# Optimization experiments

Hardware: AMD Instinct MI355X
Metric: run time of the kernel (lower is better)

Reference implementation:

```python
import jax, jax.numpy as jnp
import numpy as np

# 24 directional shifts (dy, dx): out[h,w] = in[h-dy, w-dx], zero elsewhere.
SHIFTS = [(0,1),(0,-1),(1,0),(-1,0),(1,1),(-1,-1),(1,-1),(-1,1),
          (0,2),(0,-2),(2,0),(-2,0),(2,2),(-2,-2),(2,-2),(-2,2),
          (2,1),(1,2),(2,-1),(1,-2),(-2,1),(-1,2),(-2,-1),(-1,-2)]

def shift2d(xg, dy, dx):
    B, G, H, W = xg.shape
    pt, pb = max(dy,0), max(-dy,0)
    pl, pr = max(dx,0), max(-dx,0)
    xp = jnp.pad(xg, ((0,0),(0,0),(pt,pb),(pl,pr)))
    return xp[:, :, pb:pb+H, pr:pr+W]

def mul_shift(x4, gamma=1.0/24.0):
    B, C, H, W = x4.shape
    g = int(C * gamma)
    parts = [shift2d(x4[:, i*g:(i+1)*g], dy, dx) for i, (dy, dx) in enumerate(SHIFTS)]
    parts.append(x4[:, 24*g:])
    return jnp.concatenate(parts, axis=1)

def zigzag_indices(h, w, start='top-left', direction='horizontal'):
    if start == 'top-left':   row_start, col_start, row_step, col_step = 0, 0, 1, 1
    elif start == 'top-right': row_start, col_start, row_step, col_step = 0, w-1, 1, -1
    elif start == 'bottom-left': row_start, col_start, row_step, col_step = h-1, 0, -1, 1
    else:                     row_start, col_start, row_step, col_step = h-1, w-1, -1, -1
    idx = []
    for i in range(h):
        r = row_start + row_step * i
        if direction == 'horizontal':
            cols = range(w) if r % 2 == 0 else range(w-1, -1, -1)
            idx += [r * w + c for c in cols]
        else:
            cc = col_start + col_step * i
            rows = range(h) if cc % 2 == 0 else range(h-1, -1, -1)
            idx += [rr * w + cc for rr in rows]
    return np.asarray(idx, dtype=np.int32)

def wkv(w, u, k, v):
    """Numerically stable RWKV WKV recurrence. w,u:(C,) k,v:(B,T,C) -> (B,T,C)."""
    B, T, C = k.shape
    def step(carry, kv):
        p, q, o = carry
        kt, vt = kv
        no = jnp.maximum(o, u + kt)
        A = jnp.exp(o - no); Bc = jnp.exp(u + kt - no)
        y = (A * p + Bc * vt) / (A * q + Bc)
        no2 = jnp.maximum(w + o, kt)
        A2 = jnp.exp(w + o - no2); B2 = jnp.exp(kt - no2)
        return (A2 * p + B2 * vt, A2 * q + B2, no2), y
    init = (jnp.zeros((B, C), k.dtype), jnp.zeros((B, C), k.dtype),
            jnp.full((B, C), -1e38, k.dtype))
    _, ys = jax.lax.scan(step, init, (jnp.swapaxes(k, 0, 1), jnp.swapaxes(v, 0, 1)))
    return jnp.swapaxes(ys, 0, 1)

def setup_inputs() -> dict:
    key = jax.random.key(0)
    ks = jax.random.split(key, 8)
    B, H, W, C = 8, 64, 64, 768
    scale = 0.02
    return {
        'x': jax.random.normal(ks[0], (B, H*W, C), jnp.float32),
        'key_w': jax.random.normal(ks[1], (C, C), jnp.float32) * scale,
        'value_w': jax.random.normal(ks[2], (C, C), jnp.float32) * scale,
        'receptance_w': jax.random.normal(ks[3], (C, C), jnp.float32) * scale,
        'output_w': jax.random.normal(ks[4], (C, C), jnp.float32) * scale,
        'spatial_decay': jax.random.normal(ks[5], (2, C), jnp.float32),
        'spatial_first': jax.random.normal(ks[6], (2, C), jnp.float32),
        'h': H, 'w': W,
    }

def reference(x, key_w, value_w, receptance_w, output_w, spatial_decay, spatial_first, h, w):
    B, T, C = x.shape
    # layer_id=0 -> scheme ('top-left','horizontal')
    order = jnp.asarray(zigzag_indices(h, w, 'top-left', 'horizontal'))
    inv = jnp.argsort(order)
    # jit_func: mul_shift in (B,C,H,W), zigzag reorder along T, projections
    x4 = jnp.transpose(x.reshape(B, h, w, C), (0, 3, 1, 2))
    x4 = mul_shift(x4)
    xs = jnp.transpose(x4.reshape(B, C, T)[:, :, order], (0, 2, 1))  # (B,T,C)
    k = xs @ key_w.T
    v = xs @ value_w.T
    sr = jax.nn.sigmoid(xs @ receptance_w.T)
    # recurrence j=0
    v = wkv(spatial_decay[0] / T, spatial_first[0] / T, k, v)
    # recurrence j=1: zigzag-permute, WKV, inverse-permute (horizontal -> same grid)
    k2 = k[:, order]
    v2 = v[:, order]
    v2 = wkv(spatial_decay[1] / T, spatial_first[1] / T, k2, v2)
    v = v2[:, inv]
    return (sr * v) @ output_w.T
```

## Files before the change

kernel.cpp:

```cpp
#include <hip/hip_runtime.h>
#include <hip/hip_bf16.h>
#include <hip/hip_fp16.h>

#define T_SEQ 4096
#define CDIM  768
#define BDIM  8
#define MROWS (BDIM * T_SEQ)
#define NKVR  (3 * CDIM)
#define CHL   64
#define NCH   (T_SEQ / CHL)
#define BC    (BDIM * CDIM)

typedef __attribute__((ext_vector_type(8))) short   short8;
typedef __attribute__((ext_vector_type(4))) float   floatx4;
typedef unsigned short ushort_t;
struct ushort4_t { ushort_t x, y, z, w; };

__device__ __forceinline__ ushort_t f2b(float f) {
    __hip_bfloat16 h = __float2bfloat16(f);
    return *(ushort_t*)&h;
}
__device__ __forceinline__ float b2f(ushort_t s) {
    __hip_bfloat16 h;
    *(ushort_t*)&h = s;
    return __bfloat162float(h);
}
__device__ __forceinline__ ushort_t f2h(float f) {
    __half h = __float2half(f);
    return *(ushort_t*)&h;
}
__device__ __forceinline__ float h2f(ushort_t s) {
    __half h;
    *(ushort_t*)&h = s;
    return __half2float(h);
}

__device__ __forceinline__ void gload_lds16(const void* g, void* l) {
    __builtin_amdgcn_global_load_lds(
        (const __attribute__((address_space(1))) void*)g,
        (__attribute__((address_space(3))) void*)l, 16, 0, 0);
}

__constant__ int c_dy[24] = {0,0,1,-1,1,-1,1,-1,0,0,2,-2,2,-2,2,-2,2,1,2,1,-2,-1,-2,-1};
__constant__ int c_dx[24] = {1,-1,0,0,1,-1,-1,1,2,-2,0,0,2,-2,-2,2,1,2,-1,-2,1,2,-1,-2};

__global__ void cvt_weights(const float* __restrict__ kw, const float* __restrict__ vw,
                            const float* __restrict__ rw, const float* __restrict__ ow,
                            ushort_t* __restrict__ wkvr, ushort_t* __restrict__ wo) {
    int i = blockIdx.x * 256 + threadIdx.x;
    if (i < CDIM * CDIM) {
        wkvr[i]                   = f2b(kw[i]);
        wkvr[i + CDIM * CDIM]     = f2b(vw[i]);
        wkvr[i + 2 * CDIM * CDIM] = f2b(rw[i]);
        wo[i]                     = f2b(ow[i]);
    }
}

__global__ void shift_zigzag(const float* __restrict__ x, ushort_t* __restrict__ xs) {
    size_t i = (size_t)blockIdx.x * 256 + threadIdx.x;
    if (i >= (size_t)MROWS * (CDIM / 4)) return;
    int c4 = (int)(i % (CDIM / 4)) * 4;
    size_t bt = i / (CDIM / 4);
    int tz = (int)(bt % T_SEQ);
    int b  = (int)(bt / T_SEQ);
    int r = tz >> 6, pos = tz & 63;
    int xcol = (r & 1) ? (63 - pos) : pos;
    int g = c4 >> 5;
    int ys = r - c_dy[g];
    int xsrc = xcol - c_dx[g];
    float4 val = {0.f, 0.f, 0.f, 0.f};
    if ((unsigned)ys < 64u && (unsigned)xsrc < 64u)
        val = *(const float4*)(x + ((size_t)b * T_SEQ + (size_t)(ys * 64 + xsrc)) * CDIM + c4);
    ushort4_t o;
    o.x = f2b(val.x); o.y = f2b(val.y); o.z = f2b(val.z); o.w = f2b(val.w);
    *(ushort4_t*)(xs + bt * CDIM + c4) = o;
}

template <int MODE, int NB>
__global__ __launch_bounds__(256, 3) void gemm_bt(
    const ushort_t* __restrict__ A, const ushort_t* __restrict__ Bw,
    ushort_t* __restrict__ out_k, ushort_t* __restrict__ out_v,
    ushort_t* __restrict__ out_sr, float* __restrict__ out_f) {
    __shared__ ushort_t As[128 * 32];
    __shared__ ushort_t Bs[128 * 32];
    const int p    = blockIdx.x;
    const int xcd  = p & 7;
    const int s    = p >> 3;
    const int mb   = xcd + 8 * (s / NB);
    const int nb   = s % NB;
    const int m0   = mb * 128;
    const int n0   = nb * 128;
    const int t    = threadIdx.x;
    const int lane = t & 63;
    const int wv   = t >> 6;
    const int wm   = (wv & 1) * 64;
    const int wn   = (wv >> 1) * 64;
    const int srow = t >> 2;
    const int skc  = (t & 3) ^ ((srow >> 1) & 3);
    const int kb   = skc * 8;
    const int l15  = lane & 15;
    const int l4   = lane >> 4;

    floatx4 acc[4][4];
#pragma unroll
    for (int i = 0; i < 4; i++)
#pragma unroll
        for (int j = 0; j < 4; j++) acc[i][j] = (floatx4){0.f, 0.f, 0.f, 0.f};

    for (int kk = 0; kk < CDIM; kk += 32) {
        __syncthreads();
        gload_lds16(A  + (size_t)(m0 + srow)      * CDIM + kk + kb, (void*)(As + t * 8));
        gload_lds16(A  + (size_t)(m0 + 64 + srow) * CDIM + kk + kb, (void*)(As + 2048 + t * 8));
        gload_lds16(Bw + (size_t)(n0 + srow)      * CDIM + kk + kb, (void*)(Bs + t * 8));
        gload_lds16(Bw + (size_t)(n0 + 64 + srow) * CDIM + kk + kb, (void*)(Bs + 2048 + t * 8));
        __syncthreads();
        short8 af[4], bfv[4];
#pragma unroll
        for (int mi = 0; mi < 4; mi++) {
            int ra = wm + mi * 16 + l15;
            af[mi] = *(const short8*)(As + ra * 32 + ((l4 ^ ((ra >> 1) & 3)) << 3));
        }
#pragma unroll
        for (int ni = 0; ni < 4; ni++) {
            int rb = wn + ni * 16 + l15;
            bfv[ni] = *(const short8*)(Bs + rb * 32 + ((l4 ^ ((rb >> 1) & 3)) << 3));
        }
#pragma unroll
        for (int mi = 0; mi < 4; mi++)
#pragma unroll
            for (int ni = 0; ni < 4; ni++)
                acc[mi][ni] = __builtin_amdgcn_mfma_f32_16x16x32_bf16(
                    af[mi], bfv[ni], acc[mi][ni], 0, 0, 0);
    }

    const int region = (MODE == 0) ? (nb / 6) : 0;
    ushort_t* outh = (region == 0) ? out_k : (region == 1) ? out_v : out_sr;
    const int ncb = n0 - region * CDIM;
#pragma unroll
    for (int mi = 0; mi < 4; mi++) {
#pragma unroll
        for (int ni = 0; ni < 4; ni++) {
            int nc = ncb + wn + ni * 16 + l15;
#pragma unroll
            for (int r = 0; r < 4; r++) {
                int mg = m0 + wm + mi * 16 + l4 * 4 + r;
                float val = acc[mi][ni][r];
                if (MODE == 0) {
                    if (region < 2)
                        outh[(size_t)mg * CDIM + nc] = f2h(val);
                    else
                        outh[(size_t)mg * CDIM + nc] =
                            f2b(1.0f / (1.0f + __expf(-val)));
                } else {
                    out_f[(size_t)mg * CDIM + (n0 + wn + ni * 16 + l15)] = val;
                }
            }
        }
    }
}


__global__ __launch_bounds__(256) void wkv_chunk_sum0(
    const ushort_t* __restrict__ kbuf, const ushort_t* __restrict__ vbuf,
    const float* __restrict__ sd,
    float* __restrict__ sumP, float* __restrict__ sumQ, float* __restrict__ sumO) {
    int gid = blockIdx.x * 256 + threadIdx.x;
    int bc = gid % BC;
    int ch = gid / BC;
    int b = bc / CDIM, c = bc % CDIM;
    const float w = sd[c] * (1.0f / (float)T_SEQ);
    size_t base = (size_t)b * T_SEQ * CDIM + c + (size_t)ch * CHL * CDIM;
    float p = 0.f, q = 0.f, o = -1e38f;
#pragma unroll 4
    for (int i = 0; i < CHL; i++) {
        size_t off = base + (size_t)i * CDIM;
        float kt = h2f(kbuf[off]), vt = h2f(vbuf[off]);
        float wo_ = w + o;
        float no2 = fmaxf(wo_, kt);
        float A2 = __expf(wo_ - no2), B2 = __expf(kt - no2);
        p = A2 * p + B2 * vt;
        q = A2 * q + B2;
        o = no2;
    }
    size_t idx = (size_t)ch * BC + bc;
    sumP[idx] = p; sumQ[idx] = q; sumO[idx] = o;
}

__global__ __launch_bounds__(256) void wkv_chunk_scan(
    const float* __restrict__ sumP, const float* __restrict__ sumQ,
    const float* __restrict__ sumO,
    float* __restrict__ inP, float* __restrict__ inQ, float* __restrict__ inO,
    const float* __restrict__ sd, int pass) {
    int bc = blockIdx.x * 256 + threadIdx.x;
    if (bc >= BC) return;
    int c = bc % CDIM;
    const float w = sd[pass * CDIM + c] * (1.0f / (float)T_SEQ);
    const float Lw = w * (float)CHL;
    float p = 0.f, q = 0.f, o = -1e38f;
    for (int ch = 0; ch < NCH; ch++) {
        size_t idx = (size_t)ch * BC + bc;
        inP[idx] = p; inQ[idx] = q; inO[idx] = o;
        float Pc = sumP[idx], Qc = sumQ[idx], Oc = sumO[idx];
        float ow_ = o + Lw;
        float no = fmaxf(ow_, Oc);
        float e1 = __expf(ow_ - no), e2 = __expf(Oc - no);
        p = e1 * p + e2 * Pc;
        q = e1 * q + e2 * Qc;
        o = no;
    }
}

__global__ __launch_bounds__(256) void wkv_replay0_sum1(
    const ushort_t* __restrict__ kbuf, ushort_t* __restrict__ vbuf,
    const float* __restrict__ sd, const float* __restrict__ sf,
    const float* __restrict__ inP, const float* __restrict__ inQ,
    const float* __restrict__ inO,
    float* __restrict__ sumP, float* __restrict__ sumQ, float* __restrict__ sumO) {
    int gid = blockIdx.x * 256 + threadIdx.x;
    int bc = gid % BC;
    int ch = gid / BC;
    int b = bc / CDIM, c = bc % CDIM;
    const float w1 = sd[c] * (1.0f / (float)T_SEQ);
    const float u1 = sf[c] * (1.0f / (float)T_SEQ);
    size_t base = (size_t)b * T_SEQ * CDIM + c + (size_t)ch * CHL * CDIM;
    size_t idx = (size_t)ch * BC + bc;
    float p = inP[idx], q = inQ[idx], o = inO[idx];
    float yv[CHL];
    float kv[CHL];
#pragma unroll 4
    for (int i = 0; i < CHL; i++) {
        size_t off = base + (size_t)i * CDIM;
        float kt = h2f(kbuf[off]), vt = h2f(vbuf[off]);
        kv[i] = kt;
        float uk = u1 + kt;
        float no = fmaxf(o, uk);
        float Ae = __expf(o - no), Be = __expf(uk - no);
        float y = (Ae * p + Be * vt) / (Ae * q + Be);
        float wo_ = w1 + o;
        float no2 = fmaxf(wo_, kt);
        float A2 = __expf(wo_ - no2), B2 = __expf(kt - no2);
        p = A2 * p + B2 * vt;
        q = A2 * q + B2;
        o = no2;
        yv[i] = y;
        vbuf[off] = f2h(y);
    }
    const float w2 = sd[CDIM + c] * (1.0f / (float)T_SEQ);
    float p2 = 0.f, q2 = 0.f, o2 = -1e38f;
    if (ch & 1) {
#pragma unroll 4
        for (int i = CHL - 1; i >= 0; i--) {
            float kt = kv[i], vt = yv[i];
            float wo_ = w2 + o2;
            float no2 = fmaxf(wo_, kt);
            float A2 = __expf(wo_ - no2), B2 = __expf(kt - no2);
            p2 = A2 * p2 + B2 * vt;
            q2 = A2 * q2 + B2;
            o2 = no2;
        }
    } else {
#pragma unroll 4
        for (int i = 0; i < CHL; i++) {
            float kt = kv[i], vt = yv[i];
            float wo_ = w2 + o2;
            float no2 = fmaxf(wo_, kt);
            float A2 = __expf(wo_ - no2), B2 = __expf(kt - no2);
            p2 = A2 * p2 + B2 * vt;
            q2 = A2 * q2 + B2;
            o2 = no2;
        }
    }
    sumP[idx] = p2; sumQ[idx] = q2; sumO[idx] = o2;
}

__global__ __launch_bounds__(256) void wkv_replay1(
    const ushort_t* __restrict__ kbuf, const ushort_t* __restrict__ vbuf,
    const ushort_t* __restrict__ srb, ushort_t* __restrict__ a2,
    const float* __restrict__ sd, const float* __restrict__ sf,
    const float* __restrict__ inP, const float* __restrict__ inQ,
    const float* __restrict__ inO) {
    int gid = blockIdx.x * 256 + threadIdx.x;
    int bc = gid % BC;
    int ch = gid / BC;
    int b = bc / CDIM, c = bc % CDIM;
    const float w = sd[CDIM + c] * (1.0f / (float)T_SEQ);
    const float u = sf[CDIM + c] * (1.0f / (float)T_SEQ);
    size_t base = (size_t)b * T_SEQ * CDIM + c;
    size_t idx = (size_t)ch * BC + bc;
    float p = inP[idx], q = inQ[idx], o = inO[idx];
#pragma unroll 4
    for (int i = 0; i < CHL; i++) {
        int row = ch * CHL + ((ch & 1) ? (CHL - 1 - i) : i);
        size_t off = base + (size_t)row * CDIM;
        float kt = h2f(kbuf[off]), vt = h2f(vbuf[off]);
        float uk = u + kt;
        float no = fmaxf(o, uk);
        float Ae = __expf(o - no), Be = __expf(uk - no);
        float y = (Ae * p + Be * vt) / (Ae * q + Be);
        float wo_ = w + o;
        float no2 = fmaxf(wo_, kt);
        float A2 = __expf(wo_ - no2), B2 = __expf(kt - no2);
        p = A2 * p + B2 * vt;
        q = A2 * q + B2;
        o = no2;
        a2[off] = f2b(y * b2f(srb[off]));
    }
}

extern "C" void kernel_launch(void* const* d_in, const int* in_sizes, int n_in,
                              void* d_out, int out_size, void* d_ws, size_t ws_size,
                              hipStream_t stream) {
    (void)in_sizes; (void)n_in; (void)out_size; (void)ws_size;
    const float* x  = (const float*)d_in[0];
    const float* kw = (const float*)d_in[1];
    const float* vw = (const float*)d_in[2];
    const float* rw = (const float*)d_in[3];
    const float* ow = (const float*)d_in[4];
    const float* sd = (const float*)d_in[5];
    const float* sf = (const float*)d_in[6];
    float* out = (float*)d_out;

    char* ws = (char*)d_ws;
    size_t off = 0;
    auto alloc = [&](size_t bytes) -> void* {
        void* p = ws + off;
        off += (bytes + 255) & ~(size_t)255;
        return p;
    };
    ushort_t* xs   = (ushort_t*)alloc((size_t)MROWS * CDIM * 2);
    ushort_t* kbuf = (ushort_t*)alloc((size_t)MROWS * CDIM * 2);
    ushort_t* vbuf = (ushort_t*)alloc((size_t)MROWS * CDIM * 2);
    ushort_t* srb  = (ushort_t*)alloc((size_t)MROWS * CDIM * 2);
    ushort_t* wkvr = (ushort_t*)alloc((size_t)NKVR * CDIM * 2);
    ushort_t* wo   = (ushort_t*)alloc((size_t)CDIM * CDIM * 2);
    float*    sumP = (float*)   alloc((size_t)NCH * BC * 4);
    float*    sumQ = (float*)   alloc((size_t)NCH * BC * 4);
    float*    sumO = (float*)   alloc((size_t)NCH * BC * 4);
    float*    inP  = (float*)   alloc((size_t)NCH * BC * 4);
    float*    inQ  = (float*)   alloc((size_t)NCH * BC * 4);
    float*    inO  = (float*)   alloc((size_t)NCH * BC * 4);

    cvt_weights<<<(CDIM * CDIM + 255) / 256, 256, 0, stream>>>(kw, vw, rw, ow, wkvr, wo);
    shift_zigzag<<<(int)(((size_t)MROWS * (CDIM / 4) + 255) / 256), 256, 0, stream>>>(x, xs);
    gemm_bt<0, 18><<<(MROWS / 128) * (NKVR / 128), 256, 0, stream>>>(
        xs, wkvr, kbuf, vbuf, srb, nullptr);

    const int nwkv = NCH * BC;
    wkv_chunk_sum0<<<nwkv / 256, 256, 0, stream>>>(kbuf, vbuf, sd, sumP, sumQ, sumO);
    wkv_chunk_scan<<<(BC + 255) / 256, 256, 0, stream>>>(sumP, sumQ, sumO,
                                                         inP, inQ, inO, sd, 0);
    wkv_replay0_sum1<<<nwkv / 256, 256, 0, stream>>>(kbuf, vbuf, sd, sf,
                                                     inP, inQ, inO, sumP, sumQ, sumO);
    wkv_chunk_scan<<<(BC + 255) / 256, 256, 0, stream>>>(sumP, sumQ, sumO,
                                                         inP, inQ, inO, sd, 1);
    wkv_replay1<<<nwkv / 256, 256, 0, stream>>>(kbuf, vbuf, srb, xs,
                                                sd, sf, inP, inQ, inO);

    gemm_bt<1, 6><<<(MROWS / 128) * (CDIM / 128), 256, 0, stream>>>(
        xs, wo, nullptr, nullptr, nullptr, out);
}
```

Measured before the change: 598.9 us.

## Interleave k/v buffers, halve WKV chunk length, and deepen GEMM K-tile

Stores k and v as interleaved half pairs in one buffer so each WKV step issues a single 32-bit load instead of two 16-bit loads. It halves the chunk length to double parallelism across the chunked scans, remapping the zigzag chunk order and reversed-chunk indexing to match. The GEMM K-tile grows from 32 to 64 with a new XOR swizzle, halving the sync count per tile at the cost of more LDS per block. The longer scan loop and the new index remapping add risk of occupancy loss and ordering mistakes.

```diff
diff --git a/kernel.cpp b/kernel.cpp
--- a/kernel.cpp
+++ b/kernel.cpp
@@ -7,13 +7,14 @@
 #define BDIM  8
 #define MROWS (BDIM * T_SEQ)
 #define NKVR  (3 * CDIM)
-#define CHL   64
+#define CHL   32
 #define NCH   (T_SEQ / CHL)
 #define BC    (BDIM * CDIM)
 
 typedef __attribute__((ext_vector_type(8))) short   short8;
 typedef __attribute__((ext_vector_type(4))) float   floatx4;
 typedef unsigned short ushort_t;
+typedef unsigned int   uint_t;
 struct ushort4_t { ushort_t x, y, z, w; };
 
 __device__ __forceinline__ ushort_t f2b(float f) {
@@ -79,10 +80,10 @@
 template <int MODE, int NB>
 __global__ __launch_bounds__(256, 3) void gemm_bt(
     const ushort_t* __restrict__ A, const ushort_t* __restrict__ Bw,
-    ushort_t* __restrict__ out_k, ushort_t* __restrict__ out_v,
-    ushort_t* __restrict__ out_sr, float* __restrict__ out_f) {
-    __shared__ ushort_t As[128 * 32];
-    __shared__ ushort_t Bs[128 * 32];
+    ushort_t* __restrict__ kvb, ushort_t* __restrict__ out_sr,
+    float* __restrict__ out_f) {
+    __shared__ ushort_t As[128 * 64];
+    __shared__ ushort_t Bs[128 * 64];
     const int p    = blockIdx.x;
     const int xcd  = p & 7;
     const int s    = p >> 3;
@@ -95,9 +96,8 @@
     const int wv   = t >> 6;
     const int wm   = (wv & 1) * 64;
     const int wn   = (wv >> 1) * 64;
-    const int srow = t >> 2;
-    const int skc  = (t & 3) ^ ((srow >> 1) & 3);
-    const int kb   = skc * 8;
+    const int srow = t >> 3;
+    const int sch  = t & 7;
     const int l15  = lane & 15;
     const int l4   = lane >> 4;
 
@@ -107,34 +107,43 @@
 #pragma unroll
         for (int j = 0; j < 4; j++) acc[i][j] = (floatx4){0.f, 0.f, 0.f, 0.f};
 
-    for (int kk = 0; kk < CDIM; kk += 32) {
+    for (int kk = 0; kk < CDIM; kk += 64) {
         __syncthreads();
-        gload_lds16(A  + (size_t)(m0 + srow)      * CDIM + kk + kb, (void*)(As + t * 8));
-        gload_lds16(A  + (size_t)(m0 + 64 + srow) * CDIM + kk + kb, (void*)(As + 2048 + t * 8));
-        gload_lds16(Bw + (size_t)(n0 + srow)      * CDIM + kk + kb, (void*)(Bs + t * 8));
-        gload_lds16(Bw + (size_t)(n0 + 64 + srow) * CDIM + kk + kb, (void*)(Bs + 2048 + t * 8));
+#pragma unroll
+        for (int j = 0; j < 4; j++) {
+            const int rowA = 32 * j + srow;
+            const int gc   = sch ^ (rowA & 7);
+            gload_lds16(A  + (size_t)(m0 + rowA) * CDIM + kk + gc * 8,
+                        (void*)(As + j * 2048 + t * 8));
+            gload_lds16(Bw + (size_t)(n0 + rowA) * CDIM + kk + gc * 8,
+                        (void*)(Bs + j * 2048 + t * 8));
+        }
         __syncthreads();
-        short8 af[4], bfv[4];
-#pragma unroll
-        for (int mi = 0; mi < 4; mi++) {
-            int ra = wm + mi * 16 + l15;
-            af[mi] = *(const short8*)(As + ra * 32 + ((l4 ^ ((ra >> 1) & 3)) << 3));
+#pragma unroll
+        for (int k2 = 0; k2 < 2; k2++) {
+            short8 af[4], bfv[4];
+#pragma unroll
+            for (int mi = 0; mi < 4; mi++) {
+                int ra = wm + mi * 16 + l15;
+                int c  = k2 * 4 + l4;
+                af[mi] = *(const short8*)(As + ra * 64 + ((c ^ (ra & 7)) << 3));
+            }
+#pragma unroll
+            for (int ni = 0; ni < 4; ni++) {
+                int rb = wn + ni * 16 + l15;
+                int c  = k2 * 4 + l4;
+                bfv[ni] = *(const short8*)(Bs + rb * 64 + ((c ^ (rb & 7)) << 3));
+            }
+#pragma unroll
+            for (int mi = 0; mi < 4; mi++)
+#pragma unroll
+                for (int ni = 0; ni < 4; ni++)
+                    acc[mi][ni] = __builtin_amdgcn_mfma_f32_16x16x32_bf16(
+                        af[mi], bfv[ni], acc[mi][ni], 0, 0, 0);
         }
-#pragma unroll
-        for (int ni = 0; ni < 4; ni++) {
-            int rb = wn + ni * 16 + l15;
-            bfv[ni] = *(const short8*)(Bs + rb * 32 + ((l4 ^ ((rb >> 1) & 3)) << 3));
-        }
-#pragma unroll
-        for (int mi = 0; mi < 4; mi++)
-#pragma unroll
-            for (int ni = 0; ni < 4; ni++)
-                acc[mi][ni] = __builtin_amdgcn_mfma_f32_16x16x32_bf16(
-                    af[mi], bfv[ni], acc[mi][ni], 0, 0, 0);
     }
 
     const int region = (MODE == 0) ? (nb / 6) : 0;
-    ushort_t* outh = (region == 0) ? out_k : (region == 1) ? out_v : out_sr;
     const int ncb = n0 - region * CDIM;
 #pragma unroll
     for (int mi = 0; mi < 4; mi++) {
@@ -146,10 +155,12 @@
                 int mg = m0 + wm + mi * 16 + l4 * 4 + r;
                 float val = acc[mi][ni][r];
                 if (MODE == 0) {
-                    if (region < 2)
-                        outh[(size_t)mg * CDIM + nc] = f2h(val);
+                    if (region == 0)
+                        kvb[((size_t)mg * CDIM + nc) * 2] = f2h(val);
+                    else if (region == 1)
+                        kvb[((size_t)mg * CDIM + nc) * 2 + 1] = f2h(val);
                     else
-                        outh[(size_t)mg * CDIM + nc] =
+                        out_sr[(size_t)mg * CDIM + nc] =
                             f2b(1.0f / (1.0f + __expf(-val)));
                 } else {
                     out_f[(size_t)mg * CDIM + (n0 + wn + ni * 16 + l15)] = val;
@@ -161,20 +172,19 @@
 
 
 __global__ __launch_bounds__(256) void wkv_chunk_sum0(
-    const ushort_t* __restrict__ kbuf, const ushort_t* __restrict__ vbuf,
-    const float* __restrict__ sd,
+    const uint_t* __restrict__ kvbuf, const float* __restrict__ sd,
     float* __restrict__ sumP, float* __restrict__ sumQ, float* __restrict__ sumO) {
     int gid = blockIdx.x * 256 + threadIdx.x;
     int bc = gid % BC;
     int ch = gid / BC;
     int b = bc / CDIM, c = bc % CDIM;
     const float w = sd[c] * (1.0f / (float)T_SEQ);
-    size_t base = (size_t)b * T_SEQ * CDIM + c + (size_t)ch * CHL * CDIM;
+    const uint_t* kv = kvbuf + ((size_t)b * T_SEQ + ch * CHL) * CDIM + c;
     float p = 0.f, q = 0.f, o = -1e38f;
-#pragma unroll 4
+#pragma unroll 8
     for (int i = 0; i < CHL; i++) {
-        size_t off = base + (size_t)i * CDIM;
-        float kt = h2f(kbuf[off]), vt = h2f(vbuf[off]);
+        uint_t u = kv[(size_t)i * CDIM];
+        float kt = h2f((ushort_t)(u & 0xffff)), vt = h2f((ushort_t)(u >> 16));
         float wo_ = w + o;
         float no2 = fmaxf(wo_, kt);
         float A2 = __expf(wo_ - no2), B2 = __expf(kt - no2);
@@ -211,7 +221,7 @@
 }
 
 __global__ __launch_bounds__(256) void wkv_replay0_sum1(
-    const ushort_t* __restrict__ kbuf, ushort_t* __restrict__ vbuf,
+    uint_t* __restrict__ kvbuf,
     const float* __restrict__ sd, const float* __restrict__ sf,
     const float* __restrict__ inP, const float* __restrict__ inQ,
     const float* __restrict__ inO,
@@ -222,16 +232,16 @@
     int b = bc / CDIM, c = bc % CDIM;
     const float w1 = sd[c] * (1.0f / (float)T_SEQ);
     const float u1 = sf[c] * (1.0f / (float)T_SEQ);
-    size_t base = (size_t)b * T_SEQ * CDIM + c + (size_t)ch * CHL * CDIM;
+    uint_t* kv = kvbuf + ((size_t)b * T_SEQ + ch * CHL) * CDIM + c;
     size_t idx = (size_t)ch * BC + bc;
     float p = inP[idx], q = inQ[idx], o = inO[idx];
     float yv[CHL];
-    float kv[CHL];
-#pragma unroll 4
+    float kvk[CHL];
+#pragma unroll
     for (int i = 0; i < CHL; i++) {
-        size_t off = base + (size_t)i * CDIM;
-        float kt = h2f(kbuf[off]), vt = h2f(vbuf[off]);
-        kv[i] = kt;
+        uint_t u = kv[(size_t)i * CDIM];
+        float kt = h2f((ushort_t)(u & 0xffff)), vt = h2f((ushort_t)(u >> 16));
+        kvk[i] = kt;
         float uk = u1 + kt;
         float no = fmaxf(o, uk);
         float Ae = __expf(o - no), Be = __expf(uk - no);
@@ -243,38 +253,28 @@
         q = A2 * q + B2;
         o = no2;
         yv[i] = y;
-        vbuf[off] = f2h(y);
+        ((ushort_t*)&kv[(size_t)i * CDIM])[1] = f2h(y);
     }
     const float w2 = sd[CDIM + c] * (1.0f / (float)T_SEQ);
     float p2 = 0.f, q2 = 0.f, o2 = -1e38f;
-    if (ch & 1) {
-#pragma unroll 4
-        for (int i = CHL - 1; i >= 0; i--) {
-            float kt = kv[i], vt = yv[i];
-            float wo_ = w2 + o2;
-            float no2 = fmaxf(wo_, kt);
-            float A2 = __expf(wo_ - no2), B2 = __expf(kt - no2);
-            p2 = A2 * p2 + B2 * vt;
-            q2 = A2 * q2 + B2;
-            o2 = no2;
-        }
-    } else {
-#pragma unroll 4
-        for (int i = 0; i < CHL; i++) {
-            float kt = kv[i], vt = yv[i];
-            float wo_ = w2 + o2;
-            float no2 = fmaxf(wo_, kt);
-            float A2 = __expf(wo_ - no2), B2 = __expf(kt - no2);
-            p2 = A2 * p2 + B2 * vt;
-            q2 = A2 * q2 + B2;
-            o2 = no2;
-        }
-    }
-    sumP[idx] = p2; sumQ[idx] = q2; sumO[idx] = o2;
+    const bool rev = (ch >> 1) & 1;
+#pragma unroll
+    for (int j = 0; j < CHL; j++) {
+        int i = rev ? (CHL - 1 - j) : j;
+        float kt = kvk[i], vt = yv[i];
+        float wo_ = w2 + o2;
+        float no2 = fmaxf(wo_, kt);
+        float A2 = __expf(wo_ - no2), B2 = __expf(kt - no2);
+        p2 = A2 * p2 + B2 * vt;
+        q2 = A2 * q2 + B2;
+        o2 = no2;
+    }
+    size_t idx2 = (size_t)((ch & 2) ? (ch ^ 1) : ch) * BC + bc;
+    sumP[idx2] = p2; sumQ[idx2] = q2; sumO[idx2] = o2;
 }
 
 __global__ __launch_bounds__(256) void wkv_replay1(
-    const ushort_t* __restrict__ kbuf, const ushort_t* __restrict__ vbuf,
+    const uint_t* __restrict__ kvbuf,
     const ushort_t* __restrict__ srb, ushort_t* __restrict__ a2,
     const float* __restrict__ sd, const float* __restrict__ sf,
     const float* __restrict__ inP, const float* __restrict__ inQ,
@@ -288,11 +288,15 @@
     size_t base = (size_t)b * T_SEQ * CDIM + c;
     size_t idx = (size_t)ch * BC + bc;
     float p = inP[idx], q = inQ[idx], o = inO[idx];
-#pragma unroll 4
+    const int r = ch >> 1;
+    const int pos0 = (ch & 1) * CHL;
+#pragma unroll 8
     for (int i = 0; i < CHL; i++) {
-        int row = ch * CHL + ((ch & 1) ? (CHL - 1 - i) : i);
-        size_t off = base + (size_t)row * CDIM;
-        float kt = h2f(kbuf[off]), vt = h2f(vbuf[off]);
+        int pos = pos0 + i;
+        int col = (r & 1) ? (63 - pos) : pos;
+        size_t off = base + (size_t)(r * 64 + col) * CDIM;
+        uint_t uu = kvbuf[off];
+        float kt = h2f((ushort_t)(uu & 0xffff)), vt = h2f((ushort_t)(uu >> 16));
         float uk = u + kt;
         float no = fmaxf(o, uk);
         float Ae = __expf(o - no), Be = __expf(uk - no);
@@ -328,8 +332,7 @@
         return p;
     };
     ushort_t* xs   = (ushort_t*)alloc((size_t)MROWS * CDIM * 2);
-    ushort_t* kbuf = (ushort_t*)alloc((size_t)MROWS * CDIM * 2);
-    ushort_t* vbuf = (ushort_t*)alloc((size_t)MROWS * CDIM * 2);
+    ushort_t* kvb  = (ushort_t*)alloc((size_t)MROWS * CDIM * 4);
     ushort_t* srb  = (ushort_t*)alloc((size_t)MROWS * CDIM * 2);
     ushort_t* wkvr = (ushort_t*)alloc((size_t)NKVR * CDIM * 2);
     ushort_t* wo   = (ushort_t*)alloc((size_t)CDIM * CDIM * 2);
@@ -343,19 +346,19 @@
     cvt_weights<<<(CDIM * CDIM + 255) / 256, 256, 0, stream>>>(kw, vw, rw, ow, wkvr, wo);
     shift_zigzag<<<(int)(((size_t)MROWS * (CDIM / 4) + 255) / 256), 256, 0, stream>>>(x, xs);
     gemm_bt<0, 18><<<(MROWS / 128) * (NKVR / 128), 256, 0, stream>>>(
-        xs, wkvr, kbuf, vbuf, srb, nullptr);
+        xs, wkvr, kvb, srb, nullptr);
 
     const int nwkv = NCH * BC;
-    wkv_chunk_sum0<<<nwkv / 256, 256, 0, stream>>>(kbuf, vbuf, sd, sumP, sumQ, sumO);
+    wkv_chunk_sum0<<<nwkv / 256, 256, 0, stream>>>((uint_t*)kvb, sd, sumP, sumQ, sumO);
     wkv_chunk_scan<<<(BC + 255) / 256, 256, 0, stream>>>(sumP, sumQ, sumO,
                                                          inP, inQ, inO, sd, 0);
-    wkv_replay0_sum1<<<nwkv / 256, 256, 0, stream>>>(kbuf, vbuf, sd, sf,
+    wkv_replay0_sum1<<<nwkv / 256, 256, 0, stream>>>((uint_t*)kvb, sd, sf,
                                                      inP, inQ, inO, sumP, sumQ, sumO);
     wkv_chunk_scan<<<(BC + 255) / 256, 256, 0, stream>>>(sumP, sumQ, sumO,
                                                          inP, inQ, inO, sd, 1);
-    wkv_replay1<<<nwkv / 256, 256, 0, stream>>>(kbuf, vbuf, srb, xs,
+    wkv_replay1<<<nwkv / 256, 256, 0, stream>>>((uint_t*)kvb, srb, xs,
                                                 sd, sf, inP, inQ, inO);
 
     gemm_bt<1, 6><<<(MROWS / 128) * (CDIM / 128), 256, 0, stream>>>(
-        xs, wo, nullptr, nullptr, nullptr, out);
-}
+        xs, wo, nullptr, nullptr, out);
+}
```

After: 571.1 us. 1.05x faster.
